# Performance work log

Hardware: AMD Instinct MI355X
Metric: run time of the kernel (lower is better)

Reference implementation:

```python
import jax, jax.numpy as jnp
import numpy as np

N = 100000   # nodes
E = 1200000  # edges
B = 64       # graphs
IN_DIM, HID, OUT_DIM = 128, 64, 2
N_HIDDEN = 2  # num_layers - 1 hidden GCN layers
EPS = 1e-5


def setup_inputs() -> dict:
    key = jax.random.key(0)
    ks = jax.random.split(key, 12)
    x = jax.random.normal(ks[0], (N, IN_DIM), dtype=jnp.float32)
    edge_index = jax.random.randint(ks[1], (2, E), 0, N, dtype=jnp.int64)
    batch = jnp.sort(jax.random.randint(ks[2], (N,), 0, B, dtype=jnp.int64))
    # Glorot-ish init for GCN linear weights (stored as [in, out])
    W_in = jax.random.normal(ks[3], (IN_DIM, HID), dtype=jnp.float32) / np.sqrt(IN_DIM)
    b_in = jnp.zeros((HID,), dtype=jnp.float32)
    W_h = jax.random.normal(ks[4], (N_HIDDEN, HID, HID), dtype=jnp.float32) / np.sqrt(HID)
    b_h = jnp.zeros((N_HIDDEN, HID), dtype=jnp.float32)
    W_out = jax.random.normal(ks[5], (HID, OUT_DIM), dtype=jnp.float32) / np.sqrt(HID)
    b_out = jnp.zeros((OUT_DIM,), dtype=jnp.float32)
    bn_gamma = jnp.ones((3, HID), dtype=jnp.float32)   # num_layers batch norms
    bn_beta = jnp.zeros((3, HID), dtype=jnp.float32)
    return {"x": x, "W_in": W_in, "b_in": b_in, "W_h": W_h, "b_h": b_h,
            "W_out": W_out, "b_out": b_out, "bn_gamma": bn_gamma,
            "bn_beta": bn_beta, "edge_index": edge_index, "batch": batch}


def _gcn_conv(h, W, b, src, dst, dinv):
    # PyG GCNConv: h' = D^-1/2 (A + I) D^-1/2 (h W) + b
    h = h @ W
    norm = dinv[src] * dinv[dst]                       # [E]
    agg = jax.ops.segment_sum(h[src] * norm[:, None], dst, num_segments=N)
    agg = agg + h * (dinv * dinv)[:, None]             # self-loop term
    return agg + b


def _batchnorm(h, gamma, beta):
    m = h.mean(axis=0)
    v = h.var(axis=0)  # biased, matches torch BN normalization
    return (h - m) * jax.lax.rsqrt(v + EPS) * gamma + beta


def reference(x, W_in, b_in, W_h, b_h, W_out, b_out, bn_gamma, bn_beta, edge_index, batch):
    src, dst = edge_index[0], edge_index[1]
    # degree with self-loops (edge weight 1)
    deg = jax.ops.segment_sum(jnp.ones((E,), x.dtype), dst, num_segments=N) + 1.0
    dinv = deg ** -0.5

    h = jax.nn.relu(_gcn_conv(x, W_in, b_in, src, dst, dinv))
    h = _batchnorm(h, bn_gamma[0], bn_beta[0])
    for i in range(N_HIDDEN):
        res = h
        h = jax.nn.relu(_gcn_conv(h, W_h[i], b_h[i], src, dst, dinv))
        h = _batchnorm(h, bn_gamma[i + 1], bn_beta[i + 1])
        h = h + res  # shapes match (HID == HID)
    h = _gcn_conv(h, W_out, b_out, src, dst, dinv)

    # global mean pool over batch segments
    sums = jax.ops.segment_sum(h, batch, num_segments=B)
    cnt = jax.ops.segment_sum(jnp.ones((N,), h.dtype), batch, num_segments=B)
    return sums / jnp.maximum(cnt, 1.0)[:, None]
```

## Files before the change

kernel.cpp:

```cpp
#include <hip/hip_runtime.h>


#define NN 100000
#define NE 1200000
#define NBATCH 64
#define IND 128
#define HID 64
#define EPSF 1e-5f
#define NBUCK 782
#define NPB 128

__global__ void k_ehist(const int* __restrict__ dst, int* __restrict__ gbh) {
  __shared__ int lh[NBUCK];
  int tid = threadIdx.x;
  for (int i = tid; i < NBUCK; i += 256) lh[i] = 0;
  __syncthreads();
  int base = blockIdx.x * 4096;
#pragma unroll
  for (int j = 0; j < 16; j++) {
    int e = base + j * 256 + tid;
    if (e < NE) atomicAdd(&lh[dst[e] >> 7], 1);
  }
  __syncthreads();
  for (int i = tid; i < NBUCK; i += 256) {
    int v = lh[i];
    if (v) atomicAdd(&gbh[i], v);
  }
}

__global__ void k_escan(const int* __restrict__ gbh, int* __restrict__ bbase,
                        int* __restrict__ bcur) {
  __shared__ int a[256];
  int tid = threadIdx.x;
  int loc[4];
  int tsum = 0;
  for (int j = 0; j < 4; j++) {
    int idx = tid * 4 + j;
    int v = (idx < NBUCK) ? gbh[idx] : 0;
    loc[j] = tsum;
    tsum += v;
  }
  a[tid] = tsum;
  __syncthreads();
  for (int off = 1; off < 256; off <<= 1) {
    int v = (tid >= off) ? a[tid - off] : 0;
    __syncthreads();
    a[tid] += v;
    __syncthreads();
  }
  int excl = a[tid] - tsum;
  for (int j = 0; j < 4; j++) {
    int idx = tid * 4 + j;
    if (idx < NBUCK) {
      int v = excl + loc[j];
      bbase[idx] = v;
      bcur[idx] = v;
    }
  }
  if (tid == 255) bbase[NBUCK] = a[255];
}

__global__ void k_escatter(const int* __restrict__ src, const int* __restrict__ dst,
                           int* __restrict__ bcur, unsigned long long* __restrict__ ebuf) {
  __shared__ int lh[NBUCK];
  __shared__ int lbase[NBUCK];
  int tid = threadIdx.x;
  for (int i = tid; i < NBUCK; i += 256) lh[i] = 0;
  __syncthreads();
  int base = blockIdx.x * 4096;
  int sv[16], dv[16], rk[16];
#pragma unroll
  for (int j = 0; j < 16; j++) {
    int e = base + j * 256 + tid;
    if (e < NE) {
      sv[j] = src[e];
      dv[j] = dst[e];
      rk[j] = atomicAdd(&lh[dv[j] >> 7], 1);
    } else {
      dv[j] = -1;
    }
  }
  __syncthreads();
  for (int i = tid; i < NBUCK; i += 256) {
    int v = lh[i];
    lbase[i] = v ? atomicAdd(&bcur[i], v) : 0;
  }
  __syncthreads();
#pragma unroll
  for (int j = 0; j < 16; j++) {
    if (dv[j] >= 0) {
      int b = dv[j] >> 7;
      ebuf[lbase[b] + rk[j]] =
          (unsigned long long)(unsigned)sv[j] | ((unsigned long long)(unsigned)dv[j] << 32);
    }
  }
}

__global__ void k_bucket_csr(const unsigned long long* __restrict__ ebuf,
                             const int* __restrict__ bbase, int* __restrict__ deg,
                             int* __restrict__ rowp, float* __restrict__ dinv,
                             int* __restrict__ col) {
  __shared__ int ldeg[NPB];
  __shared__ int lcur[NPB];
  __shared__ int sred[NPB];
  int b = blockIdx.x, tid = threadIdx.x;
  int nbase = b * NPB;
  int e0 = bbase[b], e1 = bbase[b + 1];
  if (tid < NPB) ldeg[tid] = 0;
  __syncthreads();
  for (int e = e0 + tid; e < e1; e += 256) {
    int d = (int)(ebuf[e] >> 32) - nbase;
    atomicAdd(&ldeg[d], 1);
  }
  __syncthreads();
  if (tid < NPB) sred[tid] = ldeg[tid];
  __syncthreads();
  for (int off = 1; off < NPB; off <<= 1) {
    int v = 0;
    if (tid < NPB && tid >= off) v = sred[tid - off];
    __syncthreads();
    if (tid < NPB) sred[tid] += v;
    __syncthreads();
  }
  if (tid < NPB) {
    int excl = sred[tid] - ldeg[tid];
    lcur[tid] = excl;
    int gn = nbase + tid;
    if (gn < NN) {
      int dg = ldeg[tid];
      deg[gn] = dg;
      rowp[gn] = e0 + excl;
      dinv[gn] = rsqrtf((float)dg + 1.0f);
    }
  }
  __syncthreads();
  for (int e = e0 + tid; e < e1; e += 256) {
    unsigned long long p = ebuf[e];
    int s = (int)(unsigned)p;
    int d = (int)(p >> 32) - nbase;
    int r = atomicAdd(&lcur[d], 1);
    col[e0 + r] = s;
  }
}

__global__ __launch_bounds__(256) void k_mmA(const float* __restrict__ X,
                                             const float* __restrict__ W,
                                             const float* __restrict__ dinv,
                                             float* __restrict__ T, int nrows) {
  __shared__ float xs[64 * 65];
  int tid = threadIdx.x;
  int rbase = blockIdx.x * 64;
  int q4 = __builtin_amdgcn_readfirstlane(tid >> 6);
  int r = tid & 63;
  int r65 = r * 65;
  float4 acc[4];
#pragma unroll
  for (int j = 0; j < 4; j++) acc[j] = {0.f, 0.f, 0.f, 0.f};

  for (int ch = 0; ch < 2; ch++) {
#pragma unroll
    for (int i = 0; i < 4; i++) {
      int f = i * 256 + tid;
      int rr = f >> 4, kq = f & 15;
      int gr = rbase + rr;
      int grc = gr < nrows ? gr : nrows - 1;
      float4 v = *(const float4*)(X + (size_t)grc * 128 + ch * 64 + 4 * kq);
      float* p = xs + rr * 65 + 4 * kq;
      p[0] = v.x; p[1] = v.y; p[2] = v.z; p[3] = v.w;
    }
    __syncthreads();
    const float* Wb = W + ch * 64 * 64 + q4 * 16;
#pragma unroll 4
    for (int k = 0; k < 64; k++) {
      float xk = xs[r65 + k];
      const float4* wr = (const float4*)(Wb + (size_t)k * 64);
#pragma unroll
      for (int j = 0; j < 4; j++) {
        float4 wv = wr[j];
        acc[j].x = fmaf(xk, wv.x, acc[j].x);
        acc[j].y = fmaf(xk, wv.y, acc[j].y);
        acc[j].z = fmaf(xk, wv.z, acc[j].z);
        acc[j].w = fmaf(xk, wv.w, acc[j].w);
      }
    }
    if (ch == 0) __syncthreads();
  }

  int row = rbase + r;
  if (row < nrows) {
    float dv = dinv[row];
    float4* t4 = (float4*)(T + (size_t)row * 64 + q4 * 16);
#pragma unroll
    for (int j = 0; j < 4; j++) {
      float4 o = acc[j];
      o.x *= dv; o.y *= dv; o.z *= dv; o.w *= dv;
      t4[j] = o;
    }
  }
}

__global__ __launch_bounds__(256) void k_mmB(const float* __restrict__ G,
                                             const double* __restrict__ st,
                                             const float* __restrict__ gamma,
                                             const float* __restrict__ beta,
                                             const float* __restrict__ res,
                                             float* __restrict__ Hside,
                                             const float* __restrict__ W,
                                             const float* __restrict__ dinv,
                                             float* __restrict__ T, int nrows) {
  __shared__ float xs[64 * 65];
  __shared__ float scl[128];
  int tid = threadIdx.x;
  if (tid < 64) {
    double m = st[tid] / (double)NN;
    double var = st[64 + tid] / (double)NN - m * m;
    float scale = gamma[tid] * rsqrtf((float)var + EPSF);
    scl[tid] = scale;
    scl[64 + tid] = beta[tid] - (float)m * scale;
  }
  __syncthreads();

  int rbase = blockIdx.x * 64;
#pragma unroll
  for (int i = 0; i < 4; i++) {
    int f = i * 256 + tid;
    int rr = f >> 4, kq = f & 15;
    int gr = rbase + rr;
    int grc = gr < nrows ? gr : nrows - 1;
    int kof = 4 * kq;
    float4 v = *(const float4*)(G + (size_t)grc * 64 + kof);
    float4 s = ((const float4*)scl)[kq];
    float4 sh = ((const float4*)(scl + 64))[kq];
    v.x = v.x * s.x + sh.x;
    v.y = v.y * s.y + sh.y;
    v.z = v.z * s.z + sh.z;
    v.w = v.w * s.w + sh.w;
    if (res != nullptr) {
      float4 rr2 = *(const float4*)(res + (size_t)grc * 64 + kof);
      v.x += rr2.x; v.y += rr2.y; v.z += rr2.z; v.w += rr2.w;
    }
    if (gr < nrows) *(float4*)(Hside + (size_t)gr * 64 + kof) = v;
    float* p = xs + rr * 65 + kof;
    p[0] = v.x; p[1] = v.y; p[2] = v.z; p[3] = v.w;
  }
  __syncthreads();

  int q4 = __builtin_amdgcn_readfirstlane(tid >> 6);
  int r = tid & 63;
  int r65 = r * 65;
  float4 acc[4];
#pragma unroll
  for (int j = 0; j < 4; j++) acc[j] = {0.f, 0.f, 0.f, 0.f};
  const float* Wb = W + q4 * 16;
#pragma unroll 4
  for (int k = 0; k < 64; k++) {
    float xk = xs[r65 + k];
    const float4* wr = (const float4*)(Wb + (size_t)k * 64);
#pragma unroll
    for (int j = 0; j < 4; j++) {
      float4 wv = wr[j];
      acc[j].x = fmaf(xk, wv.x, acc[j].x);
      acc[j].y = fmaf(xk, wv.y, acc[j].y);
      acc[j].z = fmaf(xk, wv.z, acc[j].z);
      acc[j].w = fmaf(xk, wv.w, acc[j].w);
    }
  }

  int row = rbase + r;
  if (row < nrows) {
    float dv = dinv[row];
    float4* t4 = (float4*)(T + (size_t)row * 64 + q4 * 16);
#pragma unroll
    for (int j = 0; j < 4; j++) {
      float4 o = acc[j];
      o.x *= dv; o.y *= dv; o.z *= dv; o.w *= dv;
      t4[j] = o;
    }
  }
}

__global__ void k_agg64(const float* __restrict__ T, const int* __restrict__ row_start,
                        const int* __restrict__ cnt, const int* __restrict__ col,
                        const float* __restrict__ dinv, const float* __restrict__ bias,
                        float* __restrict__ G, int relu) {
  int lane = threadIdx.x & 63;
  int wv = threadIdx.x >> 6;
  int node = blockIdx.x * 4 + wv;
  if (node >= NN) return;
  int grp = lane >> 4;
  int q = lane & 15;
  int s = row_start[node];
  int c = cnt[node];
  float4 acc = {0.f, 0.f, 0.f, 0.f};
  for (int i = 0; i < c; i += 16) {
    int j0 = i + grp, j1 = j0 + 4, j2 = j0 + 8, j3 = j0 + 12;
    int s0 = col[s + (j0 < c ? j0 : 0)];
    int s1 = col[s + (j1 < c ? j1 : 0)];
    int s2 = col[s + (j2 < c ? j2 : 0)];
    int s3 = col[s + (j3 < c ? j3 : 0)];
    float4 t0 = ((const float4*)(T + (size_t)s0 * 64))[q];
    float4 t1 = ((const float4*)(T + (size_t)s1 * 64))[q];
    float4 t2 = ((const float4*)(T + (size_t)s2 * 64))[q];
    float4 t3 = ((const float4*)(T + (size_t)s3 * 64))[q];
    float w0 = j0 < c ? 1.f : 0.f;
    float w1 = j1 < c ? 1.f : 0.f;
    float w2 = j2 < c ? 1.f : 0.f;
    float w3 = j3 < c ? 1.f : 0.f;
    acc.x = fmaf(w0, t0.x, acc.x); acc.y = fmaf(w0, t0.y, acc.y);
    acc.z = fmaf(w0, t0.z, acc.z); acc.w = fmaf(w0, t0.w, acc.w);
    acc.x = fmaf(w1, t1.x, acc.x); acc.y = fmaf(w1, t1.y, acc.y);
    acc.z = fmaf(w1, t1.z, acc.z); acc.w = fmaf(w1, t1.w, acc.w);
    acc.x = fmaf(w2, t2.x, acc.x); acc.y = fmaf(w2, t2.y, acc.y);
    acc.z = fmaf(w2, t2.z, acc.z); acc.w = fmaf(w2, t2.w, acc.w);
    acc.x = fmaf(w3, t3.x, acc.x); acc.y = fmaf(w3, t3.y, acc.y);
    acc.z = fmaf(w3, t3.z, acc.z); acc.w = fmaf(w3, t3.w, acc.w);
  }
  acc.x += __shfl_xor(acc.x, 16, 64);
  acc.y += __shfl_xor(acc.y, 16, 64);
  acc.z += __shfl_xor(acc.z, 16, 64);
  acc.w += __shfl_xor(acc.w, 16, 64);
  acc.x += __shfl_xor(acc.x, 32, 64);
  acc.y += __shfl_xor(acc.y, 32, 64);
  acc.z += __shfl_xor(acc.z, 32, 64);
  acc.w += __shfl_xor(acc.w, 32, 64);
  if (grp == 0) {
    float di = dinv[node];
    float4 ts = ((const float4*)(T + (size_t)node * 64))[q];
    float4 bs = ((const float4*)bias)[q];
    float4 o;
    o.x = (acc.x + ts.x) * di + bs.x;
    o.y = (acc.y + ts.y) * di + bs.y;
    o.z = (acc.z + ts.z) * di + bs.z;
    o.w = (acc.w + ts.w) * di + bs.w;
    if (relu) {
      o.x = fmaxf(o.x, 0.f);
      o.y = fmaxf(o.y, 0.f);
      o.z = fmaxf(o.z, 0.f);
      o.w = fmaxf(o.w, 0.f);
    }
    ((float4*)(G + (size_t)node * 64))[q] = o;
  }
}

__global__ __launch_bounds__(256) void k_stats(const float* __restrict__ H,
                                               double* __restrict__ st) {
  int q = threadIdx.x & 15;
  int rg = threadIdx.x >> 4;
  float4 s1 = {0.f, 0.f, 0.f, 0.f};
  float4 s2 = {0.f, 0.f, 0.f, 0.f};
  for (int r = blockIdx.x * 16 + rg; r < NN; r += gridDim.x * 16) {
    float4 v = *(const float4*)(H + (size_t)r * 64 + q * 4);
    s1.x += v.x; s1.y += v.y; s1.z += v.z; s1.w += v.w;
    s2.x = fmaf(v.x, v.x, s2.x); s2.y = fmaf(v.y, v.y, s2.y);
    s2.z = fmaf(v.z, v.z, s2.z); s2.w = fmaf(v.w, v.w, s2.w);
  }
  __shared__ float a[16][16][8];
  a[rg][q][0] = s1.x; a[rg][q][1] = s1.y; a[rg][q][2] = s1.z; a[rg][q][3] = s1.w;
  a[rg][q][4] = s2.x; a[rg][q][5] = s2.y; a[rg][q][6] = s2.z; a[rg][q][7] = s2.w;
  __syncthreads();
  int tid = threadIdx.x;
  if (tid < 128) {
    int f = tid & 63;
    int which = tid >> 6;
    int qq = f >> 2, jj = (f & 3) + which * 4;
    float t = 0.f;
#pragma unroll
    for (int g = 0; g < 16; g++) t += a[g][qq][jj];
    unsafeAtomicAdd(&st[which * 64 + f], (double)t);
  }
}

__global__ void k_bnmmout(const float* __restrict__ G, const double* __restrict__ st,
                          const float* __restrict__ gamma, const float* __restrict__ beta,
                          const float* __restrict__ res, const float* __restrict__ W,
                          const float* __restrict__ dinv, float* __restrict__ T2,
                          int nrows) {
  __shared__ float Wl[128];
  __shared__ float scl[128];
  int tid = threadIdx.x;
  if (tid < 32) ((float4*)Wl)[tid] = ((const float4*)W)[tid];
  else if (tid >= 64 && tid < 128) {
    int f = tid - 64;
    double m = st[f] / (double)NN;
    double var = st[64 + f] / (double)NN - m * m;
    float scale = gamma[f] * rsqrtf((float)var + EPSF);
    scl[f] = scale;
    scl[64 + f] = beta[f] - (float)m * scale;
  }
  __syncthreads();
  int row = blockIdx.x * 256 + tid;
  if (row >= nrows) return;
  const float4* g4 = (const float4*)(G + (size_t)row * 64);
  const float4* r4 = (const float4*)(res + (size_t)row * 64);
  float a0 = 0.f, a1 = 0.f;
#pragma unroll
  for (int q = 0; q < 16; q++) {
    float4 v = g4[q];
    float4 rr = r4[q];
    float4 s = ((const float4*)scl)[q];
    float4 sh = ((const float4*)(scl + 64))[q];
    float h0 = v.x * s.x + sh.x + rr.x;
    float h1 = v.y * s.y + sh.y + rr.y;
    float h2 = v.z * s.z + sh.z + rr.z;
    float h3 = v.w * s.w + sh.w + rr.w;
    const float* wk = Wl + q * 8;
    a0 = fmaf(h0, wk[0], a0); a1 = fmaf(h0, wk[1], a1);
    a0 = fmaf(h1, wk[2], a0); a1 = fmaf(h1, wk[3], a1);
    a0 = fmaf(h2, wk[4], a0); a1 = fmaf(h2, wk[5], a1);
    a0 = fmaf(h3, wk[6], a0); a1 = fmaf(h3, wk[7], a1);
  }
  float dv = dinv[row];
  T2[(size_t)row * 2 + 0] = a0 * dv;
  T2[(size_t)row * 2 + 1] = a1 * dv;
}

__global__ void k_agg2pool(const float* __restrict__ T2, const int* __restrict__ rowp,
                           const int* __restrict__ cnt, const int* __restrict__ col,
                           const float* __restrict__ dinv, const float* __restrict__ bias,
                           const int* __restrict__ batch, float* __restrict__ pool,
                           int* __restrict__ pcnt, int* __restrict__ tick,
                           float* __restrict__ out, int nblk) {
  __shared__ float pl[128];
  __shared__ int pc[64];
  __shared__ int lastflag;
  int tid = threadIdx.x;
  if (tid < 128) pl[tid] = 0.f;
  if (tid < 64) pc[tid] = 0;
  __syncthreads();
  int node = blockIdx.x * 256 + tid;
  if (node < NN) {
    int s = rowp[node];
    int c = cnt[node];
    float a0 = 0.f, a1 = 0.f;
    for (int i = 0; i < c; i += 4) {
      int j0 = i, j1 = i + 1, j2 = i + 2, j3 = i + 3;
      int s0 = col[s + j0];
      int sA = col[s + (j1 < c ? j1 : j0)];
      int sB = col[s + (j2 < c ? j2 : j0)];
      int sC = col[s + (j3 < c ? j3 : j0)];
      float2 t0 = *(const float2*)(T2 + 2 * (size_t)s0);
      float2 t1 = *(const float2*)(T2 + 2 * (size_t)sA);
      float2 t2 = *(const float2*)(T2 + 2 * (size_t)sB);
      float2 t3 = *(const float2*)(T2 + 2 * (size_t)sC);
      float w1 = j1 < c ? 1.f : 0.f;
      float w2 = j2 < c ? 1.f : 0.f;
      float w3 = j3 < c ? 1.f : 0.f;
      a0 += t0.x; a1 += t0.y;
      a0 = fmaf(w1, t1.x, a0); a1 = fmaf(w1, t1.y, a1);
      a0 = fmaf(w2, t2.x, a0); a1 = fmaf(w2, t2.y, a1);
      a0 = fmaf(w3, t3.x, a0); a1 = fmaf(w3, t3.y, a1);
    }
    float di = dinv[node];
    float2 tn = *(const float2*)(T2 + 2 * (size_t)node);
    float v0 = (a0 + tn.x) * di + bias[0];
    float v1 = (a1 + tn.y) * di + bias[1];
    int bb = batch[node];
    atomicAdd(&pl[bb * 2 + 0], v0);
    atomicAdd(&pl[bb * 2 + 1], v1);
    atomicAdd(&pc[bb], 1);
  }
  __syncthreads();
  if (tid < 128 && pl[tid] != 0.f) unsafeAtomicAdd(&pool[tid], pl[tid]);
  if (tid < 64 && pc[tid] != 0) atomicAdd(&pcnt[tid], pc[tid]);
  __syncthreads();
  if (tid == 0) {
    __threadfence();
    int old = atomicAdd(tick, 1);
    lastflag = (old == nblk - 1) ? 1 : 0;
  }
  __syncthreads();
  if (lastflag && tid < 128) {
    float v = unsafeAtomicAdd(&pool[tid], 0.f);
    int c = atomicAdd(&pcnt[tid >> 1], 0);
    out[tid] = v / (float)(c > 0 ? c : 1);
  }
}

extern "C" void kernel_launch(void* const* d_in, const int* in_sizes, int n_in,
                              void* d_out, int out_size, void* d_ws, size_t ws_size,
                              hipStream_t stream) {
  (void)in_sizes; (void)n_in; (void)out_size; (void)ws_size;
  const float* x     = (const float*)d_in[0];
  const float* W_in  = (const float*)d_in[1];
  const float* b_in  = (const float*)d_in[2];
  const float* W_h   = (const float*)d_in[3];
  const float* b_h   = (const float*)d_in[4];
  const float* W_out = (const float*)d_in[5];
  const float* b_out = (const float*)d_in[6];
  const float* gamma = (const float*)d_in[7];
  const float* beta  = (const float*)d_in[8];
  const int*   ei    = (const int*)d_in[9];
  const int*   batch = (const int*)d_in[10];
  const int* src = ei;
  const int* dst = ei + NE;
  float* out = (float*)d_out;

  char* w = (char*)d_ws;
  size_t off = 0;
  auto alloc = [&](size_t bytes) -> void* {
    void* p = (void*)(w + off);
    off += (bytes + 511) & ~(size_t)511;
    return p;
  };
  int*    deg   = (int*)alloc((size_t)NN * 4);
  int*    rowp  = (int*)alloc((size_t)NN * 4);
  int*    col   = (int*)alloc((size_t)NE * 4);
  float*  dinv  = (float*)alloc((size_t)NN * 4);
  int*    bbase = (int*)alloc((NBUCK + 1) * 4);
  int*    bcur  = (int*)alloc(NBUCK * 4);
  char*   zzone = (char*)alloc(7680);
  double* stats = (double*)zzone;
  float*  pool  = (float*)(zzone + 3072);
  int*    pcnt  = (int*)(zzone + 3584);
  int*    tick  = (int*)(zzone + 3840);
  int*    gbh   = (int*)(zzone + 4096);
  float*  buf0  = (float*)alloc((size_t)NN * HID * 4);
  float*  buf1  = (float*)alloc((size_t)NN * HID * 4);
  float*  buf2  = (float*)alloc((size_t)NN * HID * 4);
  float*  T2    = (float*)alloc((size_t)NN * 2 * 4);
  unsigned long long* ebuf = (unsigned long long*)buf0;

  hipMemsetAsync(zzone, 0, 7424, stream);

  k_ehist<<<293, 256, 0, stream>>>(dst, gbh);
  k_escan<<<1, 256, 0, stream>>>(gbh, bbase, bcur);
  k_escatter<<<293, 256, 0, stream>>>(src, dst, bcur, ebuf);
  k_bucket_csr<<<NBUCK, 256, 0, stream>>>(ebuf, bbase, deg, rowp, dinv, col);

  const int mmgrid = (NN + 63) / 64;

  k_mmA<<<mmgrid, 256, 0, stream>>>(x, W_in, dinv, buf0, NN);
  k_agg64<<<(NN + 3) / 4, 256, 0, stream>>>(buf0, rowp, deg, col, dinv, b_in, buf1, 1);
  k_stats<<<512, 256, 0, stream>>>(buf1, stats);

  k_mmB<<<mmgrid, 256, 0, stream>>>(buf1, stats, gamma, beta, nullptr, buf2, W_h,
                                    dinv, buf0, NN);
  k_agg64<<<(NN + 3) / 4, 256, 0, stream>>>(buf0, rowp, deg, col, dinv, b_h, buf1, 1);
  k_stats<<<512, 256, 0, stream>>>(buf1, stats + 128);

  k_mmB<<<mmgrid, 256, 0, stream>>>(buf1, stats + 128, gamma + 64, beta + 64, buf2,
                                    buf0, W_h + HID * HID, dinv, buf1, NN);
  k_agg64<<<(NN + 3) / 4, 256, 0, stream>>>(buf1, rowp, deg, col, dinv, b_h + HID, buf2, 1);
  k_stats<<<512, 256, 0, stream>>>(buf2, stats + 256);

  k_bnmmout<<<(NN + 255) / 256, 256, 0, stream>>>(buf2, stats + 256, gamma + 128,
                                                  beta + 128, buf0, W_out, dinv, T2, NN);
  const int pgrid = (NN + 255) / 256;
  k_agg2pool<<<pgrid, 256, 0, stream>>>(T2, rowp, deg, col, dinv, b_out, batch, pool,
                                        pcnt, tick, out, pgrid);
}
```

Baseline: 438.9 us.

## Reorder hidden GCN layers to aggregate first, then fuse matmul into aggregation

New measurement: 450.5 us. 1.03x slower.

```diff
diff --git a/kernel.cpp b/kernel.cpp
--- a/kernel.cpp
+++ b/kernel.cpp
@@ -99,7 +99,7 @@
 __global__ void k_bucket_csr(const unsigned long long* __restrict__ ebuf,
                              const int* __restrict__ bbase, int* __restrict__ deg,
                              int* __restrict__ rowp, float* __restrict__ dinv,
-                             int* __restrict__ col) {
+                             float* __restrict__ rd, int* __restrict__ col) {
   __shared__ int ldeg[NPB];
   __shared__ int lcur[NPB];
   __shared__ int sred[NPB];
@@ -131,6 +131,7 @@
       deg[gn] = dg;
       rowp[gn] = e0 + excl;
       dinv[gn] = rsqrtf((float)dg + 1.0f);
+      rd[gn] = sqrtf((float)dg + 1.0f);
     }
   }
   __syncthreads();
@@ -184,86 +185,6 @@
       }
     }
     if (ch == 0) __syncthreads();
-  }
-
-  int row = rbase + r;
-  if (row < nrows) {
-    float dv = dinv[row];
-    float4* t4 = (float4*)(T + (size_t)row * 64 + q4 * 16);
-#pragma unroll
-    for (int j = 0; j < 4; j++) {
-      float4 o = acc[j];
-      o.x *= dv; o.y *= dv; o.z *= dv; o.w *= dv;
-      t4[j] = o;
-    }
-  }
-}
-
-__global__ __launch_bounds__(256) void k_mmB(const float* __restrict__ G,
-                                             const double* __restrict__ st,
-                                             const float* __restrict__ gamma,
-                                             const float* __restrict__ beta,
-                                             const float* __restrict__ res,
-                                             float* __restrict__ Hside,
-                                             const float* __restrict__ W,
-                                             const float* __restrict__ dinv,
-                                             float* __restrict__ T, int nrows) {
-  __shared__ float xs[64 * 65];
-  __shared__ float scl[128];
-  int tid = threadIdx.x;
-  if (tid < 64) {
-    double m = st[tid] / (double)NN;
-    double var = st[64 + tid] / (double)NN - m * m;
-    float scale = gamma[tid] * rsqrtf((float)var + EPSF);
-    scl[tid] = scale;
-    scl[64 + tid] = beta[tid] - (float)m * scale;
-  }
-  __syncthreads();
-
-  int rbase = blockIdx.x * 64;
-#pragma unroll
-  for (int i = 0; i < 4; i++) {
-    int f = i * 256 + tid;
-    int rr = f >> 4, kq = f & 15;
-    int gr = rbase + rr;
-    int grc = gr < nrows ? gr : nrows - 1;
-    int kof = 4 * kq;
-    float4 v = *(const float4*)(G + (size_t)grc * 64 + kof);
-    float4 s = ((const float4*)scl)[kq];
-    float4 sh = ((const float4*)(scl + 64))[kq];
-    v.x = v.x * s.x + sh.x;
-    v.y = v.y * s.y + sh.y;
-    v.z = v.z * s.z + sh.z;
-    v.w = v.w * s.w + sh.w;
-    if (res != nullptr) {
-      float4 rr2 = *(const float4*)(res + (size_t)grc * 64 + kof);
-      v.x += rr2.x; v.y += rr2.y; v.z += rr2.z; v.w += rr2.w;
-    }
-    if (gr < nrows) *(float4*)(Hside + (size_t)gr * 64 + kof) = v;
-    float* p = xs + rr * 65 + kof;
-    p[0] = v.x; p[1] = v.y; p[2] = v.z; p[3] = v.w;
-  }
-  __syncthreads();
-
-  int q4 = __builtin_amdgcn_readfirstlane(tid >> 6);
-  int r = tid & 63;
-  int r65 = r * 65;
-  float4 acc[4];
-#pragma unroll
-  for (int j = 0; j < 4; j++) acc[j] = {0.f, 0.f, 0.f, 0.f};
-  const float* Wb = W + q4 * 16;
-#pragma unroll 4
-  for (int k = 0; k < 64; k++) {
-    float xk = xs[r65 + k];
-    const float4* wr = (const float4*)(Wb + (size_t)k * 64);
-#pragma unroll
-    for (int j = 0; j < 4; j++) {
-      float4 wv = wr[j];
-      acc[j].x = fmaf(xk, wv.x, acc[j].x);
-      acc[j].y = fmaf(xk, wv.y, acc[j].y);
-      acc[j].z = fmaf(xk, wv.z, acc[j].z);
-      acc[j].w = fmaf(xk, wv.w, acc[j].w);
-    }
   }
 
   int row = rbase + r;
@@ -342,6 +263,116 @@
   }
 }
 
+__global__ __launch_bounds__(256) void k_bnapply(const float* __restrict__ G,
+                                                 const double* __restrict__ st,
+                                                 const float* __restrict__ gamma,
+                                                 const float* __restrict__ beta,
+                                                 const float* __restrict__ resS,
+                                                 const float* __restrict__ dinv,
+                                                 float* __restrict__ Hs) {
+  __shared__ float scl[128];
+  int tid = threadIdx.x;
+  if (tid < 64) {
+    double m = st[tid] / (double)NN;
+    double var = st[64 + tid] / (double)NN - m * m;
+    float scale = gamma[tid] * rsqrtf((float)var + EPSF);
+    scl[tid] = scale;
+    scl[64 + tid] = beta[tid] - (float)m * scale;
+  }
+  __syncthreads();
+  int idx = blockIdx.x * 256 + tid;
+  if (idx >= NN * 16) return;
+  int r = idx >> 4, kq = idx & 15;
+  float4 v = ((const float4*)G)[idx];
+  float4 s = ((const float4*)scl)[kq];
+  float4 sh = ((const float4*)(scl + 64))[kq];
+  float di = dinv[r];
+  v.x = (v.x * s.x + sh.x) * di;
+  v.y = (v.y * s.y + sh.y) * di;
+  v.z = (v.z * s.z + sh.z) * di;
+  v.w = (v.w * s.w + sh.w) * di;
+  if (resS != nullptr) {
+    float4 rr = ((const float4*)resS)[idx];
+    v.x += rr.x; v.y += rr.y; v.z += rr.z; v.w += rr.w;
+  }
+  ((float4*)Hs)[idx] = v;
+}
+
+__global__ __launch_bounds__(256) void k_aggmm(const float* __restrict__ Hs,
+                                               const int* __restrict__ row_start,
+                                               const int* __restrict__ cnt,
+                                               const int* __restrict__ col,
+                                               const float* __restrict__ dinv,
+                                               const float* __restrict__ bias,
+                                               const float* __restrict__ W,
+                                               float* __restrict__ G) {
+  __shared__ float Wl[64 * 64];
+  __shared__ float vL[4][64];
+  int tid = threadIdx.x;
+#pragma unroll
+  for (int i = 0; i < 4; i++)
+    ((float4*)Wl)[i * 256 + tid] = ((const float4*)W)[i * 256 + tid];
+
+  int lane = tid & 63;
+  int wv = tid >> 6;
+  int node = blockIdx.x * 4 + wv;
+  int grp = lane >> 4;
+  int q = lane & 15;
+  int s = row_start[node];
+  int c = cnt[node];
+  float4 acc = {0.f, 0.f, 0.f, 0.f};
+  for (int i = 0; i < c; i += 16) {
+    int j0 = i + grp, j1 = j0 + 4, j2 = j0 + 8, j3 = j0 + 12;
+    int s0 = col[s + (j0 < c ? j0 : 0)];
+    int s1 = col[s + (j1 < c ? j1 : 0)];
+    int s2 = col[s + (j2 < c ? j2 : 0)];
+    int s3 = col[s + (j3 < c ? j3 : 0)];
+    float4 t0 = ((const float4*)(Hs + (size_t)s0 * 64))[q];
+    float4 t1 = ((const float4*)(Hs + (size_t)s1 * 64))[q];
+    float4 t2 = ((const float4*)(Hs + (size_t)s2 * 64))[q];
+    float4 t3 = ((const float4*)(Hs + (size_t)s3 * 64))[q];
+    float w0 = j0 < c ? 1.f : 0.f;
+    float w1 = j1 < c ? 1.f : 0.f;
+    float w2 = j2 < c ? 1.f : 0.f;
+    float w3 = j3 < c ? 1.f : 0.f;
+    acc.x = fmaf(w0, t0.x, acc.x); acc.y = fmaf(w0, t0.y, acc.y);
+    acc.z = fmaf(w0, t0.z, acc.z); acc.w = fmaf(w0, t0.w, acc.w);
+    acc.x = fmaf(w1, t1.x, acc.x); acc.y = fmaf(w1, t1.y, acc.y);
+    acc.z = fmaf(w1, t1.z, acc.z); acc.w = fmaf(w1, t1.w, acc.w);
+    acc.x = fmaf(w2, t2.x, acc.x); acc.y = fmaf(w2, t2.y, acc.y);
+    acc.z = fmaf(w2, t2.z, acc.z); acc.w = fmaf(w2, t2.w, acc.w);
+    acc.x = fmaf(w3, t3.x, acc.x); acc.y = fmaf(w3, t3.y, acc.y);
+    acc.z = fmaf(w3, t3.z, acc.z); acc.w = fmaf(w3, t3.w, acc.w);
+  }
+  acc.x += __shfl_xor(acc.x, 16, 64);
+  acc.y += __shfl_xor(acc.y, 16, 64);
+  acc.z += __shfl_xor(acc.z, 16, 64);
+  acc.w += __shfl_xor(acc.w, 16, 64);
+  acc.x += __shfl_xor(acc.x, 32, 64);
+  acc.y += __shfl_xor(acc.y, 32, 64);
+  acc.z += __shfl_xor(acc.z, 32, 64);
+  acc.w += __shfl_xor(acc.w, 32, 64);
+  if (grp == 0) {
+    float di = dinv[node];
+    float4 ts = ((const float4*)(Hs + (size_t)node * 64))[q];
+    float4 v;
+    v.x = (acc.x + ts.x) * di;
+    v.y = (acc.y + ts.y) * di;
+    v.z = (acc.z + ts.z) * di;
+    v.w = (acc.w + ts.w) * di;
+    ((float4*)vL[wv])[q] = v;
+  }
+  __syncthreads();
+
+  const float* vw = vL[wv];
+  float y = 0.f;
+#pragma unroll 8
+  for (int k = 0; k < 64; k++) y = fmaf(vw[k], Wl[k * 64 + lane], y);
+  y += bias[lane];
+  y = fmaxf(y, 0.f);
+  G[(size_t)node * 64 + lane] = y;
+}
+
 __global__ __launch_bounds__(256) void k_stats(const float* __restrict__ H,
                                                double* __restrict__ st) {
   int q = threadIdx.x & 15;
@@ -372,9 +403,9 @@
 
 __global__ void k_bnmmout(const float* __restrict__ G, const double* __restrict__ st,
                           const float* __restrict__ gamma, const float* __restrict__ beta,
-                          const float* __restrict__ res, const float* __restrict__ W,
-                          const float* __restrict__ dinv, float* __restrict__ T2,
-                          int nrows) {
+                          const float* __restrict__ resS, const float* __restrict__ W,
+                          const float* __restrict__ dinv, const float* __restrict__ rd,
+                          float* __restrict__ T2, int nrows) {
   __shared__ float Wl[128];
   __shared__ float scl[128];
   int tid = threadIdx.x;
@@ -391,7 +422,8 @@
   int row = blockIdx.x * 256 + tid;
   if (row >= nrows) return;
   const float4* g4 = (const float4*)(G + (size_t)row * 64);
-  const float4* r4 = (const float4*)(res + (size_t)row * 64);
+  const float4* r4 = (const float4*)(resS + (size_t)row * 64);
+  float rdv = rd[row];
   float a0 = 0.f, a1 = 0.f;
 #pragma unroll
   for (int q = 0; q < 16; q++) {
@@ -399,10 +431,10 @@
     float4 rr = r4[q];
     float4 s = ((const float4*)scl)[q];
     float4 sh = ((const float4*)(scl + 64))[q];
-    float h0 = v.x * s.x + sh.x + rr.x;
-    float h1 = v.y * s.y + sh.y + rr.y;
-    float h2 = v.z * s.z + sh.z + rr.z;
-    float h3 = v.w * s.w + sh.w + rr.w;
+    float h0 = v.x * s.x + sh.x + rr.x * rdv;
+    float h1 = v.y * s.y + sh.y + rr.y * rdv;
+    float h2 = v.z * s.z + sh.z + rr.z * rdv;
+    float h3 = v.w * s.w + sh.w + rr.w * rdv;
     const float* wk = Wl + q * 8;
     a0 = fmaf(h0, wk[0], a0); a1 = fmaf(h0, wk[1], a1);
     a0 = fmaf(h1, wk[2], a0); a1 = fmaf(h1, wk[3], a1);
@@ -506,6 +538,7 @@
   int*    rowp  = (int*)alloc((size_t)NN * 4);
   int*    col   = (int*)alloc((size_t)NE * 4);
   float*  dinv  = (float*)alloc((size_t)NN * 4);
+  float*  rdeg  = (float*)alloc((size_t)NN * 4);
   int*    bbase = (int*)alloc((NBUCK + 1) * 4);
   int*    bcur  = (int*)alloc(NBUCK * 4);
   char*   zzone = (char*)alloc(7680);
@@ -525,26 +558,29 @@
   k_ehist<<<293, 256, 0, stream>>>(dst, gbh);
   k_escan<<<1, 256, 0, stream>>>(gbh, bbase, bcur);
   k_escatter<<<293, 256, 0, stream>>>(src, dst, bcur, ebuf);
-  k_bucket_csr<<<NBUCK, 256, 0, stream>>>(ebuf, bbase, deg, rowp, dinv, col);
+  k_bucket_csr<<<NBUCK, 256, 0, stream>>>(ebuf, bbase, deg, rowp, dinv, rdeg, col);
 
   const int mmgrid = (NN + 63) / 64;
+  const int agrid = NN / 4;
+  const int bngrid = (NN * 16 + 255) / 256;
 
   k_mmA<<<mmgrid, 256, 0, stream>>>(x, W_in, dinv, buf0, NN);
-  k_agg64<<<(NN + 3) / 4, 256, 0, stream>>>(buf0, rowp, deg, col, dinv, b_in, buf1, 1);
+  k_agg64<<<agrid, 256, 0, stream>>>(buf0, rowp, deg, col, dinv, b_in, buf1, 1);
   k_stats<<<512, 256, 0, stream>>>(buf1, stats);
 
-  k_mmB<<<mmgrid, 256, 0, stream>>>(buf1, stats, gamma, beta, nullptr, buf2, W_h,
-                                    dinv, buf0, NN);
-  k_agg64<<<(NN + 3) / 4, 256, 0, stream>>>(buf0, rowp, deg, col, dinv, b_h, buf1, 1);
-  k_stats<<<512, 256, 0, stream>>>(buf1, stats + 128);
-
-  k_mmB<<<mmgrid, 256, 0, stream>>>(buf1, stats + 128, gamma + 64, beta + 64, buf2,
-                                    buf0, W_h + HID * HID, dinv, buf1, NN);
-  k_agg64<<<(NN + 3) / 4, 256, 0, stream>>>(buf1, rowp, deg, col, dinv, b_h + HID, buf2, 1);
+  k_bnapply<<<bngrid, 256, 0, stream>>>(buf1, stats, gamma, beta, nullptr, dinv, buf2);
+  k_aggmm<<<agrid, 256, 0, stream>>>(buf2, rowp, deg, col, dinv, b_h, W_h, buf0);
+  k_stats<<<512, 256, 0, stream>>>(buf0, stats + 128);
+
+  k_bnapply<<<bngrid, 256, 0, stream>>>(buf0, stats + 128, gamma + 64, beta + 64,
+                                        buf2, dinv, buf1);
+  k_aggmm<<<agrid, 256, 0, stream>>>(buf1, rowp, deg, col, dinv, b_h + HID,
+                                     W_h + HID * HID, buf2);
   k_stats<<<512, 256, 0, stream>>>(buf2, stats + 256);
 
   k_bnmmout<<<(NN + 255) / 256, 256, 0, stream>>>(buf2, stats + 256, gamma + 128,
-                                                  beta + 128, buf0, W_out, dinv, T2, NN);
+                                                  beta + 128, buf1, W_out, dinv, rdeg,
+                                                  T2, NN);
   const int pgrid = (NN + 255) / 256;
   k_agg2pool<<<pgrid, 256, 0, stream>>>(T2, rowp, deg, col, dinv, b_out, batch, pool,
                                         pcnt, tick, out, pgrid);
```
